# Optimization experiments

Hardware: AMD Instinct MI355X
Metric: run time of the kernel (lower is better)

The kernel has to match this reference:

```python
import jax, jax.numpy as jnp
import numpy as np


def setup_inputs() -> dict:
    key = jax.random.key(0)
    ks = jax.random.split(key, 9)
    bs, F, T, d_in, Nh, d_out = 4, 8, 256, 64, 8, 64
    std = 2.0  # gaussian_init_delta_std
    return {
        "X": jax.random.normal(ks[0], (bs, F, T, d_in), dtype=jnp.float32),
        "attention_center": std * jax.random.normal(ks[1], (F, Nh, 1), dtype=jnp.float32),
        "alpha": jax.random.normal(ks[2], (F,), dtype=jnp.float32),
        "W_query": jax.random.normal(ks[3], (F, T, d_in, Nh, 2), dtype=jnp.float32),
        "W_key": jax.random.normal(ks[4], (F, T, d_in, Nh, 2), dtype=jnp.float32),
        "Wkey_": jax.random.normal(ks[5], (F, 2, 2), dtype=jnp.float32),
        "u": jax.random.normal(ks[6], (F, T, 2), dtype=jnp.float32),
        "W": jax.random.normal(ks[7], (F, Nh * d_in, d_out), dtype=jnp.float32),
        "b": jax.random.normal(ks[8], (F, T, d_out), dtype=jnp.float32),
    }


def reference(X, attention_center, alpha, W_query, W_key, Wkey_, u, W, b):
    bs, F, T, d_in = X.shape
    Nh = W_query.shape[3]

    # relative-position features R[t,l] = (l-t)^2, (l-t); identical across F in the original
    rel = (jnp.arange(T)[None, :] - jnp.arange(T)[:, None]).astype(jnp.float32)
    R = jnp.stack([rel ** 2, rel], axis=-1)  # (T,T,2)

    query = jnp.einsum('bftd,ftdhe->bfthe', X, W_query)  # (bs,F,T,Nh,2)
    key = jnp.einsum('bftd,ftdhe->bfthe', X, W_key)      # (bs,F,T,Nh,2)

    r_delta = jnp.einsum('fde,tle->ftld', Wkey_, R)      # (F,T,T,2)

    centers = jnp.concatenate([jnp.ones_like(attention_center), -2.0 * attention_center], axis=-1)  # (F,Nh,2)
    v = -alpha[:, None, None] * centers                  # (F,Nh,2)

    scores = (
        jnp.einsum('bfthe,bflhe->bfthl', query, key)
        + jnp.einsum('bfthe,ftle->bfthl', query, r_delta)
        + jnp.einsum('fle,bfthe->bfthl', u, key)
        + jnp.einsum('fhe,ftle->fthl', v, r_delta)[None]
    )  # (bs,F,T,Nh,T)

    probs = jax.nn.softmax(scores, axis=-1)

    vals = jnp.einsum('bfthl,bfld->bfthd', probs, X)     # (bs,F,T,Nh,d_in)
    vals = vals.reshape(bs, F, T, Nh * d_in)

    return jnp.einsum('bftd,fdo->bfto', vals, W) + b     # (bs,F,T,d_out)
```

## Files before the change

kernel.cpp:

```cpp
#include <hip/hip_runtime.h>
#include <hip/hip_bf16.h>

#define BS 4
#define NF 8
#define NT 256
#define DIN 64
#define NH 8
#define DOUT 64
#define TT 8
#define MROWS 64
#define NCHUNK 32

typedef unsigned short u16;
typedef __attribute__((ext_vector_type(8))) short short8;
typedef __attribute__((ext_vector_type(4))) float f32x4;
typedef __attribute__((ext_vector_type(4))) unsigned int u32x4;

static __device__ __forceinline__ u16 f2bf(float x) {
    __hip_bfloat16 h = __float2bfloat16(x);
    u16 r; __builtin_memcpy(&r, &h, 2); return r;
}
static __device__ __forceinline__ unsigned pk2(float a, float b) {
    return (unsigned)f2bf(a) | ((unsigned)f2bf(b) << 16);
}

__global__ __launch_bounds__(256) void prep_kernel(
    const float* __restrict__ X,
    const float* __restrict__ Wq,
    const float* __restrict__ Wk,
    const float* __restrict__ W,
    float* __restrict__ q,
    float* __restrict__ k,
    u16* __restrict__ XT,
    u16* __restrict__ Wt)
{
    __shared__ float sT[64][65];
    const int tid = threadIdx.x;
    const int bid = blockIdx.x;

    if (bid < 2048) {
        const int ft = bid;
        const int f = ft >> 8, t = ft & 255;
        const int dsp   = tid & 7;
        const int heq   = (tid >> 3) & 3;
        const int b     = (tid >> 5) & 3;
        const int which = tid >> 7;

        const float* xp = X + (((size_t)((b * NF + f) * NT + t)) << 6) + (dsp << 3);
        float4 x0 = *(const float4*)xp;
        float4 x1 = *(const float4*)(xp + 4);

        const float* wmat = which ? Wk : Wq;
        const float* wp = wmat + ((size_t)ft << 10) + ((dsp << 3) << 4) + (heq << 2);

        float4 a = {0.f, 0.f, 0.f, 0.f};
        float xs[8] = {x0.x, x0.y, x0.z, x0.w, x1.x, x1.y, x1.z, x1.w};
        #pragma unroll
        for (int j = 0; j < 8; ++j) {
            float4 w4 = *(const float4*)(wp + (j << 4));
            a.x = fmaf(xs[j], w4.x, a.x);
            a.y = fmaf(xs[j], w4.y, a.y);
            a.z = fmaf(xs[j], w4.z, a.z);
            a.w = fmaf(xs[j], w4.w, a.w);
        }
        #pragma unroll
        for (int off = 1; off < 8; off <<= 1) {
            a.x += __shfl_xor(a.x, off);
            a.y += __shfl_xor(a.y, off);
            a.z += __shfl_xor(a.z, off);
            a.w += __shfl_xor(a.w, off);
        }
        if (dsp == 0) {
            float* outp = which ? k : q;
            *(float4*)(outp + (((size_t)((b * NF + f) * NT + t)) << 4) + (heq << 2)) = a;
        }
    } else if (bid < 2080) {
        const int bf = bid - 2048;
        for (int lc = 0; lc < 4; ++lc) {
            #pragma unroll
            for (int i = 0; i < 16; ++i) {
                int l = i * 4 + (tid >> 6), d = tid & 63;
                sT[l][d] = X[(((size_t)(bf * NT) + lc * 64 + l) << 6) + d];
            }
            __syncthreads();
            #pragma unroll
            for (int i = 0; i < 16; ++i) {
                int d = i * 4 + (tid >> 6), l = tid & 63;
                XT[(((size_t)(bf * 64) + d) << 8) + lc * 64 + l] = f2bf(sT[l][d]);
            }
            __syncthreads();
        }
    } else {
        const int idx = bid - 2080;
        const int f = idx >> 3, kc = idx & 7;
        #pragma unroll
        for (int i = 0; i < 16; ++i) {
            int kk = i * 4 + (tid >> 6), o = tid & 63;
            sT[kk][o] = W[(((size_t)(f * 512) + kc * 64 + kk) << 6) + o];
        }
        __syncthreads();
        #pragma unroll
        for (int i = 0; i < 16; ++i) {
            int o = i * 4 + (tid >> 6), kk = tid & 63;
            Wt[(((size_t)(f * 64) + o) << 9) + kc * 64 + kk] = f2bf(sT[kk][o]);
        }
    }
}

__global__ __launch_bounds__(256, 2) void attn_kernel(
    const float* __restrict__ ac,
    const float* __restrict__ alpha,
    const float* __restrict__ Wkey_,
    const float* __restrict__ u,
    const float* __restrict__ bias,
    const float* __restrict__ q,
    const float* __restrict__ kws,
    const u16* __restrict__ XT,
    const u16* __restrict__ Wt,
    float* __restrict__ out)
{
    __shared__ u16  sP[MROWS * 256];
    __shared__ float sKU[4608];
    __shared__ float sC[MROWS * 8];
    __shared__ float sRed[4 * MROWS];
    __shared__ float sInvS[MROWS];

    const int tid = threadIdx.x;
    const int bid = blockIdx.x;
    const int ch = bid & 31;
    const int f  = (bid >> 5) & 7;
    const int b  = bid >> 8;
    const int bf = b * NF + f;
    const int t0 = ch * TT;

    {
        const float4* k4 = (const float4*)(kws + ((size_t)bf << 12));
        float4* d4 = (float4*)sKU;
        #pragma unroll
        for (int i = 0; i < 4; ++i) d4[i * 256 + tid] = k4[i * 256 + tid];
        if (tid < 128) ((float4*)(sKU + 4096))[tid] = ((const float4*)(u + f * 512))[tid];
    }
    __syncthreads();
    if (tid < MROWS) {
        int m = tid, h = m & 7, t = t0 + (m >> 3);
        float q0 = q[((size_t)(bf * NT + t) << 4) + h * 2];
        float q1 = q[((size_t)(bf * NT + t) << 4) + h * 2 + 1];
        float kt0 = sKU[t * 16 + h * 2], kt1 = sKU[t * 16 + h * 2 + 1];
        float al = alpha[f];
        float a0 = q0 - al;
        float a1 = q1 + 2.f * al * ac[f * 8 + h];
        float wk0 = Wkey_[f * 4], wk1 = Wkey_[f * 4 + 1];
        float wk2 = Wkey_[f * 4 + 2], wk3 = Wkey_[f * 4 + 3];
        float* cc = sC + m * 8;
        cc[0] = q0; cc[1] = q1; cc[2] = kt0; cc[3] = kt1;
        cc[4] = a0 * wk0 + a1 * wk2;
        cc[5] = a0 * wk1 + a1 * wk3;
    }
    __syncthreads();

    const int m  = tid & 63;
    const int lq = tid >> 6;
    const int t  = t0 + (m >> 3);
    const int h  = m & 7;
    float q0, q1, kt0, kt1, c2, c1;
    {
        const float* cc = sC + m * 8;
        q0 = cc[0]; q1 = cc[1]; kt0 = cc[2]; kt1 = cc[3]; c2 = cc[4]; c1 = cc[5];
    }
    const float* sKp = sKU;
    const float* sUp = sKU + 4096;

    float mx = -1e30f;
    {
        float rel = (float)(lq * 64 - t);
        #pragma unroll 8
        for (int j = 0; j < 64; ++j) {
            int l = lq * 64 + j;
            float2 K = *(const float2*)(sKp + l * 16 + h * 2);
            float2 U = *(const float2*)(sUp + l * 2);
            float s = (c2 * rel + c1) * rel;
            s = fmaf(q0, K.x, s); s = fmaf(q1, K.y, s);
            s = fmaf(kt0, U.x, s); s = fmaf(kt1, U.y, s);
            mx = fmaxf(mx, s);
            rel += 1.f;
        }
    }
    sRed[lq * 64 + m] = mx;
    __syncthreads();
    const float M = fmaxf(fmaxf(sRed[m], sRed[64 + m]), fmaxf(sRed[128 + m], sRed[192 + m]));
    __syncthreads();

    float sum = 0.f;
    {
        float rel = (float)(lq * 64 - t);
        unsigned pk[4]; float ep = 0.f;
        #pragma unroll 8
        for (int j = 0; j < 64; ++j) {
            int l = lq * 64 + j;
            float2 K = *(const float2*)(sKp + l * 16 + h * 2);
            float2 U = *(const float2*)(sUp + l * 2);
            float s = (c2 * rel + c1) * rel;
            s = fmaf(q0, K.x, s); s = fmaf(q1, K.y, s);
            s = fmaf(kt0, U.x, s); s = fmaf(kt1, U.y, s);
            float e = __expf(s - M);
            sum += e;
            if ((j & 1) == 0) ep = e;
            else pk[(j & 7) >> 1] = pk2(ep, e);
            if ((j & 7) == 7) {
                int chunk = l >> 3;
                int phys = chunk ^ (m & 15);
                *(u32x4*)&sP[m * 256 + phys * 8] = (u32x4){pk[0], pk[1], pk[2], pk[3]};
            }
            rel += 1.f;
        }
    }
    sRed[lq * 64 + m] = sum;
    __syncthreads();
    if (tid < MROWS)
        sInvS[tid] = 1.f / ((sRed[tid] + sRed[64 + tid]) + (sRed[128 + tid] + sRed[192 + tid]));
    __syncthreads();

    const int wv   = tid >> 6;
    const int lane = tid & 63;
    const int quad = lane >> 4;
    const int ln   = lane & 15;

    f32x4 acc0 = {0.f, 0.f, 0.f, 0.f}, acc1 = acc0, acc2 = acc0, acc3 = acc0;
    const u16* xb = XT + ((size_t)bf << 14);
    #pragma unroll
    for (int ks = 0; ks < 8; ++ks) {
        int chunk = ks * 4 + quad;
        int phys = chunk ^ ln;
        short8 a = *(const short8*)&sP[(wv * 16 + ln) * 256 + phys * 8];
        int l = ks * 32 + quad * 8;
        short8 b0 = *(const short8*)(xb + (0 * 16 + ln) * 256 + l);
        short8 b1 = *(const short8*)(xb + (1 * 16 + ln) * 256 + l);
        short8 b2 = *(const short8*)(xb + (2 * 16 + ln) * 256 + l);
        short8 b3 = *(const short8*)(xb + (3 * 16 + ln) * 256 + l);
        acc0 = __builtin_amdgcn_mfma_f32_16x16x32_bf16(a, b0, acc0, 0, 0, 0);
        acc1 = __builtin_amdgcn_mfma_f32_16x16x32_bf16(a, b1, acc1, 0, 0, 0);
        acc2 = __builtin_amdgcn_mfma_f32_16x16x32_bf16(a, b2, acc2, 0, 0, 0);
        acc3 = __builtin_amdgcn_mfma_f32_16x16x32_bf16(a, b3, acc3, 0, 0, 0);
    }

    u16* sVals = (u16*)sKU;
    #pragma unroll
    for (int reg = 0; reg < 4; ++reg) {
        int mg = wv * 16 + quad * 4 + reg;
        float inv = sInvS[mg];
        int tl = mg >> 3, hh = mg & 7;
        u16* dst = sVals + tl * 520 + hh * 64 + ln;
        dst[0]  = f2bf(acc0[reg] * inv);
        dst[16] = f2bf(acc1[reg] * inv);
        dst[32] = f2bf(acc2[reg] * inv);
        dst[48] = f2bf(acc3[reg] * inv);
    }
    __syncthreads();

    f32x4 oacc = {0.f, 0.f, 0.f, 0.f};
    const u16* wb = Wt + ((size_t)(f * 64 + wv * 16 + ln) << 9);
    #pragma unroll
    for (int ks = 0; ks < 16; ++ks) {
        int k2 = ks * 32 + quad * 8;
        short8 a = *(const short8*)(sVals + ln * 520 + k2);
        short8 bw = *(const short8*)(wb + k2);
        oacc = __builtin_amdgcn_mfma_f32_16x16x32_bf16(a, bw, oacc, 0, 0, 0);
    }
    {
        int o = wv * 16 + ln;
        #pragma unroll
        for (int reg = 0; reg < 4; ++reg) {
            int tl = quad * 4 + reg;
            if (tl < TT) {
                int tg = t0 + tl;
                out[((size_t)(bf * NT + tg) << 6) + o] =
                    oacc[reg] + bias[((size_t)(f * NT + tg) << 6) + o];
            }
        }
    }
}

extern "C" void kernel_launch(void* const* d_in, const int* in_sizes, int n_in,
                              void* d_out, int out_size, void* d_ws, size_t ws_size,
                              hipStream_t stream) {
    const float* X     = (const float*)d_in[0];
    const float* ac    = (const float*)d_in[1];
    const float* alpha = (const float*)d_in[2];
    const float* Wq    = (const float*)d_in[3];
    const float* Wk    = (const float*)d_in[4];
    const float* Wkey_ = (const float*)d_in[5];
    const float* u     = (const float*)d_in[6];
    const float* W     = (const float*)d_in[7];
    const float* bb    = (const float*)d_in[8];
    float* out = (float*)d_out;

    float* qws = (float*)d_ws;
    float* kws = qws + 131072;
    u16* XT = (u16*)(kws + 131072);
    u16* Wt = XT + 524288;

    hipLaunchKernelGGL(prep_kernel, dim3(2144), dim3(256), 0, stream,
                       X, Wq, Wk, W, qws, kws, XT, Wt);
    hipLaunchKernelGGL(attn_kernel, dim3(BS * NF * NCHUNK), dim3(256), 0, stream,
                       ac, alpha, Wkey_, u, bb, qws, kws, XT, Wt, out);
}
```

Baseline: 137.7 us.

## Restructure projection and score loops, prefetch MFMA operands, raise occupancy

The Q/K projection is remapped so each wave handles one (which, f, t) pair, with 16-element dot products and a two-step cross-lane reduction. This halves the prep grid and cuts shuffle work. In the attention kernel, each thread now computes two query rows over 32 keys, so each K/U LDS load is reused twice, and per-row constants are computed in registers, dropping the sC staging and one barrier. XT and Wt operand loads for the MFMA loops are software-prefetched one step ahead, and launch bounds ask for 3 blocks per CU. The extra registers from the two-row work and the prefetches could conflict with the higher occupancy target and cause spills.

```diff
diff --git a/kernel.cpp b/kernel.cpp
--- a/kernel.cpp
+++ b/kernel.cpp
@@ -38,44 +38,43 @@
     const int tid = threadIdx.x;
     const int bid = blockIdx.x;
 
-    if (bid < 2048) {
-        const int ft = bid;
+    if (bid < 1024) {
+        const int gw = (bid << 2) + (tid >> 6);
+        const int which = gw >> 11;
+        const int ft = gw & 2047;
         const int f = ft >> 8, t = ft & 255;
-        const int dsp   = tid & 7;
-        const int heq   = (tid >> 3) & 3;
-        const int b     = (tid >> 5) & 3;
-        const int which = tid >> 7;
-
-        const float* xp = X + (((size_t)((b * NF + f) * NT + t)) << 6) + (dsp << 3);
-        float4 x0 = *(const float4*)xp;
-        float4 x1 = *(const float4*)(xp + 4);
+        const int ln = tid & 63;
+        const int dg = ln >> 4;
+        const int b  = (ln >> 2) & 3;
+        const int hq = ln & 3;
 
         const float* wmat = which ? Wk : Wq;
-        const float* wp = wmat + ((size_t)ft << 10) + ((dsp << 3) << 4) + (heq << 2);
-
-        float4 a = {0.f, 0.f, 0.f, 0.f};
-        float xs[8] = {x0.x, x0.y, x0.z, x0.w, x1.x, x1.y, x1.z, x1.w};
-        #pragma unroll
-        for (int j = 0; j < 8; ++j) {
+        const float* wp = wmat + ((size_t)ft << 10) + (dg << 8) + (hq << 2);
+        const float* xp = X + (((size_t)((b * NF + f) * NT + t)) << 6) + (dg << 4);
+
+        float4 acc = {0.f, 0.f, 0.f, 0.f};
+        #pragma unroll
+        for (int j = 0; j < 16; ++j) {
+            float xv = xp[j];
             float4 w4 = *(const float4*)(wp + (j << 4));
-            a.x = fmaf(xs[j], w4.x, a.x);
-            a.y = fmaf(xs[j], w4.y, a.y);
-            a.z = fmaf(xs[j], w4.z, a.z);
-            a.w = fmaf(xs[j], w4.w, a.w);
-        }
-        #pragma unroll
-        for (int off = 1; off < 8; off <<= 1) {
-            a.x += __shfl_xor(a.x, off);
-            a.y += __shfl_xor(a.y, off);
-            a.z += __shfl_xor(a.z, off);
-            a.w += __shfl_xor(a.w, off);
-        }
-        if (dsp == 0) {
+            acc.x = fmaf(xv, w4.x, acc.x);
+            acc.y = fmaf(xv, w4.y, acc.y);
+            acc.z = fmaf(xv, w4.z, acc.z);
+            acc.w = fmaf(xv, w4.w, acc.w);
+        }
+        #pragma unroll
+        for (int off = 16; off <= 32; off <<= 1) {
+            acc.x += __shfl_xor(acc.x, off);
+            acc.y += __shfl_xor(acc.y, off);
+            acc.z += __shfl_xor(acc.z, off);
+            acc.w += __shfl_xor(acc.w, off);
+        }
+        if (dg == 0) {
             float* outp = which ? k : q;
-            *(float4*)(outp + (((size_t)((b * NF + f) * NT + t)) << 4) + (heq << 2)) = a;
-        }
-    } else if (bid < 2080) {
-        const int bf = bid - 2048;
+            *(float4*)(outp + (((size_t)((b * NF + f) * NT + t)) << 4) + (hq << 2)) = acc;
+        }
+    } else if (bid < 1056) {
+        const int bf = bid - 1024;
         for (int lc = 0; lc < 4; ++lc) {
             #pragma unroll
             for (int i = 0; i < 16; ++i) {
@@ -91,7 +90,7 @@
             __syncthreads();
         }
     } else {
-        const int idx = bid - 2080;
+        const int idx = bid - 1056;
         const int f = idx >> 3, kc = idx & 7;
         #pragma unroll
         for (int i = 0; i < 16; ++i) {
@@ -107,7 +106,7 @@
     }
 }
 
-__global__ __launch_bounds__(256, 2) void attn_kernel(
+__global__ __launch_bounds__(256, 3) void attn_kernel(
     const float* __restrict__ ac,
     const float* __restrict__ alpha,
     const float* __restrict__ Wkey_,
@@ -121,8 +120,8 @@
 {
     __shared__ u16  sP[MROWS * 256];
     __shared__ float sKU[4608];
-    __shared__ float sC[MROWS * 8];
-    __shared__ float sRed[4 * MROWS];
+    __shared__ float sRed[8 * MROWS];
+    __shared__ float sM[MROWS];
     __shared__ float sInvS[MROWS];
 
     const int tid = threadIdx.x;
@@ -141,102 +140,131 @@
         if (tid < 128) ((float4*)(sKU + 4096))[tid] = ((const float4*)(u + f * 512))[tid];
     }
     __syncthreads();
-    if (tid < MROWS) {
-        int m = tid, h = m & 7, t = t0 + (m >> 3);
-        float q0 = q[((size_t)(bf * NT + t) << 4) + h * 2];
-        float q1 = q[((size_t)(bf * NT + t) << 4) + h * 2 + 1];
-        float kt0 = sKU[t * 16 + h * 2], kt1 = sKU[t * 16 + h * 2 + 1];
+
+    const int h  = tid & 7;
+    const int tp = (tid >> 3) & 3;
+    const int le = tid >> 5;
+    const int t_a = t0 + tp * 2, t_b = t_a + 1;
+    const int m_a = tp * 16 + h, m_b = m_a + 8;
+    const int lbase = le * 32;
+
+    float q0a, q1a, kt0a, kt1a, c2a, c1a;
+    float q0b, q1b, kt0b, kt1b, c2b, c1b;
+    {
         float al = alpha[f];
-        float a0 = q0 - al;
-        float a1 = q1 + 2.f * al * ac[f * 8 + h];
-        float wk0 = Wkey_[f * 4], wk1 = Wkey_[f * 4 + 1];
+        float acv = ac[f * 8 + h];
+        float wk0 = Wkey_[f * 4],     wk1 = Wkey_[f * 4 + 1];
         float wk2 = Wkey_[f * 4 + 2], wk3 = Wkey_[f * 4 + 3];
-        float* cc = sC + m * 8;
-        cc[0] = q0; cc[1] = q1; cc[2] = kt0; cc[3] = kt1;
-        cc[4] = a0 * wk0 + a1 * wk2;
-        cc[5] = a0 * wk1 + a1 * wk3;
-    }
-    __syncthreads();
-
-    const int m  = tid & 63;
-    const int lq = tid >> 6;
-    const int t  = t0 + (m >> 3);
-    const int h  = m & 7;
-    float q0, q1, kt0, kt1, c2, c1;
-    {
-        const float* cc = sC + m * 8;
-        q0 = cc[0]; q1 = cc[1]; kt0 = cc[2]; kt1 = cc[3]; c2 = cc[4]; c1 = cc[5];
-    }
-    const float* sKp = sKU;
-    const float* sUp = sKU + 4096;
-
-    float mx = -1e30f;
-    {
-        float rel = (float)(lq * 64 - t);
+        float2 qa = *(const float2*)(q + ((size_t)(bf * NT + t_a) << 4) + (h << 1));
+        float2 qb = *(const float2*)(q + ((size_t)(bf * NT + t_b) << 4) + (h << 1));
+        q0a = qa.x; q1a = qa.y; q0b = qb.x; q1b = qb.y;
+        kt0a = sKU[t_a * 16 + h * 2]; kt1a = sKU[t_a * 16 + h * 2 + 1];
+        kt0b = sKU[t_b * 16 + h * 2]; kt1b = sKU[t_b * 16 + h * 2 + 1];
+        float a0 = q0a - al, a1 = q1a + 2.f * al * acv;
+        c2a = a0 * wk0 + a1 * wk2; c1a = a0 * wk1 + a1 * wk3;
+        a0 = q0b - al; a1 = q1b + 2.f * al * acv;
+        c2b = a0 * wk0 + a1 * wk2; c1b = a0 * wk1 + a1 * wk3;
+    }
+
+    float mxa = -1e30f, mxb = -1e30f;
+    {
+        float rela = (float)(lbase - t_a);
         #pragma unroll 8
-        for (int j = 0; j < 64; ++j) {
-            int l = lq * 64 + j;
-            float2 K = *(const float2*)(sKp + l * 16 + h * 2);
-            float2 U = *(const float2*)(sUp + l * 2);
-            float s = (c2 * rel + c1) * rel;
-            s = fmaf(q0, K.x, s); s = fmaf(q1, K.y, s);
-            s = fmaf(kt0, U.x, s); s = fmaf(kt1, U.y, s);
-            mx = fmaxf(mx, s);
-            rel += 1.f;
-        }
-    }
-    sRed[lq * 64 + m] = mx;
-    __syncthreads();
-    const float M = fmaxf(fmaxf(sRed[m], sRed[64 + m]), fmaxf(sRed[128 + m], sRed[192 + m]));
-    __syncthreads();
-
-    float sum = 0.f;
-    {
-        float rel = (float)(lq * 64 - t);
-        unsigned pk[4]; float ep = 0.f;
+        for (int j = 0; j < 32; ++j) {
+            int l = lbase + j;
+            float2 K = *(const float2*)(sKU + l * 16 + h * 2);
+            float2 U = *(const float2*)(sKU + 4096 + l * 2);
+            float relb = rela - 1.f;
+            float sa = (c2a * rela + c1a) * rela;
+            sa = fmaf(q0a, K.x, sa); sa = fmaf(q1a, K.y, sa);
+            sa = fmaf(kt0a, U.x, sa); sa = fmaf(kt1a, U.y, sa);
+            float sb = (c2b * relb + c1b) * relb;
+            sb = fmaf(q0b, K.x, sb); sb = fmaf(q1b, K.y, sb);
+            sb = fmaf(kt0b, U.x, sb); sb = fmaf(kt1b, U.y, sb);
+            mxa = fmaxf(mxa, sa); mxb = fmaxf(mxb, sb);
+            rela += 1.f;
+        }
+    }
+    sRed[le * 64 + m_a] = mxa;
+    sRed[le * 64 + m_b] = mxb;
+    __syncthreads();
+    if (tid < 64) {
+        float mm = sRed[tid];
+        #pragma unroll
+        for (int i = 1; i < 8; ++i) mm = fmaxf(mm, sRed[i * 64 + tid]);
+        sM[tid] = mm;
+    }
+    __syncthreads();
+
+    {
+        const float Ma = sM[m_a], Mb = sM[m_b];
+        float suma = 0.f, sumb = 0.f;
+        float rela = (float)(lbase - t_a);
+        unsigned pka[4], pkb[4];
+        float epa = 0.f, epb = 0.f;
         #pragma unroll 8
-        for (int j = 0; j < 64; ++j) {
-            int l = lq * 64 + j;
-            float2 K = *(const float2*)(sKp + l * 16 + h * 2);
-            float2 U = *(const float2*)(sUp + l * 2);
-            float s = (c2 * rel + c1) * rel;
-            s = fmaf(q0, K.x, s); s = fmaf(q1, K.y, s);
-            s = fmaf(kt0, U.x, s); s = fmaf(kt1, U.y, s);
-            float e = __expf(s - M);
-            sum += e;
-            if ((j & 1) == 0) ep = e;
-            else pk[(j & 7) >> 1] = pk2(ep, e);
+        for (int j = 0; j < 32; ++j) {
+            int l = lbase + j;
+            float2 K = *(const float2*)(sKU + l * 16 + h * 2);
+            float2 U = *(const float2*)(sKU + 4096 + l * 2);
+            float relb = rela - 1.f;
+            float sa = (c2a * rela + c1a) * rela;
+            sa = fmaf(q0a, K.x, sa); sa = fmaf(q1a, K.y, sa);
+            sa = fmaf(kt0a, U.x, sa); sa = fmaf(kt1a, U.y, sa);
+            float sb = (c2b * relb + c1b) * relb;
+            sb = fmaf(q0b, K.x, sb); sb = fmaf(q1b, K.y, sb);
+            sb = fmaf(kt0b, U.x, sb); sb = fmaf(kt1b, U.y, sb);
+            float ea = __expf(sa - Ma), eb = __expf(sb - Mb);
+            suma += ea; sumb += eb;
+            if ((j & 1) == 0) { epa = ea; epb = eb; }
+            else { pka[(j & 7) >> 1] = pk2(epa, ea); pkb[(j & 7) >> 1] = pk2(epb, eb); }
             if ((j & 7) == 7) {
                 int chunk = l >> 3;
-                int phys = chunk ^ (m & 15);
-                *(u32x4*)&sP[m * 256 + phys * 8] = (u32x4){pk[0], pk[1], pk[2], pk[3]};
+                int pa = chunk ^ (m_a & 15), pb = chunk ^ (m_b & 15);
+                *(u32x4*)&sP[m_a * 256 + pa * 8] = (u32x4){pka[0], pka[1], pka[2], pka[3]};
+                *(u32x4*)&sP[m_b * 256 + pb * 8] = (u32x4){pkb[0], pkb[1], pkb[2], pkb[3]};
             }
-            rel += 1.f;
-        }
-    }
-    sRed[lq * 64 + m] = sum;
-    __syncthreads();
-    if (tid < MROWS)
-        sInvS[tid] = 1.f / ((sRed[tid] + sRed[64 + tid]) + (sRed[128 + tid] + sRed[192 + tid]));
-    __syncthreads();
+            rela += 1.f;
+        }
+        sRed[le * 64 + m_a] = suma;
+        sRed[le * 64 + m_b] = sumb;
+    }
 
     const int wv   = tid >> 6;
     const int lane = tid & 63;
     const int quad = lane >> 4;
     const int ln   = lane & 15;
+    const u16* xb = XT + ((size_t)bf << 14);
+    short8 nb0, nb1, nb2, nb3;
+    {
+        int l = quad * 8;
+        nb0 = *(const short8*)(xb + (0 * 16 + ln) * 256 + l);
+        nb1 = *(const short8*)(xb + (1 * 16 + ln) * 256 + l);
+        nb2 = *(const short8*)(xb + (2 * 16 + ln) * 256 + l);
+        nb3 = *(const short8*)(xb + (3 * 16 + ln) * 256 + l);
+    }
+    __syncthreads();
+    if (tid < 64) {
+        float ss = sRed[tid];
+        #pragma unroll
+        for (int i = 1; i < 8; ++i) ss += sRed[i * 64 + tid];
+        sInvS[tid] = 1.f / ss;
+    }
+    __syncthreads();
 
     f32x4 acc0 = {0.f, 0.f, 0.f, 0.f}, acc1 = acc0, acc2 = acc0, acc3 = acc0;
-    const u16* xb = XT + ((size_t)bf << 14);
     #pragma unroll
     for (int ks = 0; ks < 8; ++ks) {
-        int chunk = ks * 4 + quad;
-        int phys = chunk ^ ln;
+        short8 b0 = nb0, b1 = nb1, b2 = nb2, b3 = nb3;
+        if (ks < 7) {
+            int l = (ks + 1) * 32 + quad * 8;
+            nb0 = *(const short8*)(xb + (0 * 16 + ln) * 256 + l);
+            nb1 = *(const short8*)(xb + (1 * 16 + ln) * 256 + l);
+            nb2 = *(const short8*)(xb + (2 * 16 + ln) * 256 + l);
+            nb3 = *(const short8*)(xb + (3 * 16 + ln) * 256 + l);
+        }
+        int phys = (ks * 4 + quad) ^ ln;
         short8 a = *(const short8*)&sP[(wv * 16 + ln) * 256 + phys * 8];
-        int l = ks * 32 + quad * 8;
-        short8 b0 = *(const short8*)(xb + (0 * 16 + ln) * 256 + l);
-        short8 b1 = *(const short8*)(xb + (1 * 16 + ln) * 256 + l);
-        short8 b2 = *(const short8*)(xb + (2 * 16 + ln) * 256 + l);
-        short8 b3 = *(const short8*)(xb + (3 * 16 + ln) * 256 + l);
         acc0 = __builtin_amdgcn_mfma_f32_16x16x32_bf16(a, b0, acc0, 0, 0, 0);
         acc1 = __builtin_amdgcn_mfma_f32_16x16x32_bf16(a, b1, acc1, 0, 0, 0);
         acc2 = __builtin_amdgcn_mfma_f32_16x16x32_bf16(a, b2, acc2, 0, 0, 0);
@@ -255,15 +283,16 @@
         dst[32] = f2bf(acc2[reg] * inv);
         dst[48] = f2bf(acc3[reg] * inv);
     }
+    const u16* wb = Wt + ((size_t)(f * 64 + wv * 16 + ln) << 9);
+    short8 nw = *(const short8*)(wb + quad * 8);
     __syncthreads();
 
     f32x4 oacc = {0.f, 0.f, 0.f, 0.f};
-    const u16* wb = Wt + ((size_t)(f * 64 + wv * 16 + ln) << 9);
     #pragma unroll
     for (int ks = 0; ks < 16; ++ks) {
-        int k2 = ks * 32 + quad * 8;
-        short8 a = *(const short8*)(sVals + ln * 520 + k2);
-        short8 bw = *(const short8*)(wb + k2);
+        short8 bw = nw;
+        if (ks < 15) nw = *(const short8*)(wb + (ks + 1) * 32 + quad * 8);
+        short8 a = *(const short8*)(sVals + ln * 520 + ks * 32 + quad * 8);
         oacc = __builtin_amdgcn_mfma_f32_16x16x32_bf16(a, bw, oacc, 0, 0, 0);
     }
     {
@@ -299,7 +328,7 @@
     u16* XT = (u16*)(kws + 131072);
     u16* Wt = XT + 524288;
 
-    hipLaunchKernelGGL(prep_kernel, dim3(2144), dim3(256), 0, stream,
+    hipLaunchKernelGGL(prep_kernel, dim3(1120), dim3(256), 0, stream,
                        X, Wq, Wk, W, qws, kws, XT, Wt);
     hipLaunchKernelGGL(attn_kernel, dim3(BS * NF * NCHUNK), dim3(256), 0, stream,
                        ac, alpha, Wkey_, u, bb, qws, kws, XT, Wt, out);
```

New measurement: 135.6 us. No clear change (-1.5%).
